# Optimization experiments

Measured on AMD Instinct MI355X. Metric: run time of the kernel, lower is better.

Reference implementation:

```python
import jax, jax.numpy as jnp
import numpy as np
from jax import lax

D_MODEL = 96; D_STATE = 16; D_INNER = 192; DT_RANK = 6; K = 4
BSZ = 2; HH = 64; WW = 64


def setup_inputs() -> dict:
    key = jax.random.key(0)
    ks = jax.random.split(key, 16)
    f = lambda k, shape, s=0.02: (jax.random.normal(k, shape) * s).astype(jnp.float32)
    P = DT_RANK + 2 * D_STATE
    return {
        "x": jax.random.normal(ks[0], (BSZ, HH, WW, D_MODEL), jnp.float32),
        "W_in": f(ks[1], (2 * D_INNER, D_MODEL)),
        "b_in": jnp.zeros((2 * D_INNER,), jnp.float32),
        "conv_w": f(ks[2], (D_INNER, 1, 3, 3)),
        "conv_b": jnp.zeros((D_INNER,), jnp.float32),
        "W_xp": f(ks[3], (K * P, K * D_INNER)),
        "b_xp": jnp.zeros((K * P,), jnp.float32),
        "W_dt": f(ks[4], (K * D_INNER, K * DT_RANK)),
        "b_dt": f(ks[5], (K * D_INNER,), 0.1),
        "A_log": jax.random.normal(ks[6], (K * D_INNER, D_STATE), jnp.float32),
        "D_skip": jnp.ones((K * D_INNER,), jnp.float32),
        "dt_bias": jax.random.normal(ks[7], (K * D_INNER,), jnp.float32),
        "W_out": f(ks[8], (D_MODEL, D_INNER)),
        "b_out": jnp.zeros((D_MODEL,), jnp.float32),
        "gamma": jnp.ones((D_INNER,), jnp.float32),
        "beta": jnp.zeros((D_INNER,), jnp.float32),
    }


def cross_scan(x):
    # x: (B, D, H, W) -> (B, 4, D, L); dirs: row-major, col-major, and their reverses
    B, D, H, W = x.shape
    L = H * W
    x0 = x.reshape(B, D, L)
    x1 = jnp.swapaxes(x, 2, 3).reshape(B, D, L)
    return jnp.stack([x0, x1, x0[..., ::-1], x1[..., ::-1]], axis=1)


def cross_merge(ys):
    # ys: (B, 4, D, H, W) -> (B, D, L); inverse of cross_scan, summed
    B, Kk, D, H, W = ys.shape
    L = H * W
    yf = ys.reshape(B, Kk, D, L)
    y02 = yf[:, 0] + yf[:, 2, :, ::-1]
    y13 = yf[:, 1] + yf[:, 3, :, ::-1]
    y13 = jnp.swapaxes(y13.reshape(B, D, W, H), 2, 3).reshape(B, D, L)
    return y02 + y13


def selective_scan(u, dt, A, Bm, Cm, D_skip, dt_bias):
    # u, dt: (B,K,Dv,L); A: (K,Dv,N); Bm, Cm: (B,K,N,L); D_skip, dt_bias: (K,Dv)
    # NOTE: torch code repeats Bm/Cm across Dv; we broadcast instead (same math).
    dt = jax.nn.softplus(dt + dt_bias[None, :, :, None])
    dt_l = jnp.moveaxis(dt, -1, 0)   # (L,B,K,Dv)
    u_l = jnp.moveaxis(u, -1, 0)     # (L,B,K,Dv)
    B_l = jnp.moveaxis(Bm, -1, 0)    # (L,B,K,N)
    C_l = jnp.moveaxis(Cm, -1, 0)    # (L,B,K,N)

    def step(h, inp):
        dt_t, u_t, b_t, c_t = inp
        dA = jnp.exp(dt_t[..., None] * A[None])                 # (B,K,Dv,N)
        dBu = (dt_t * u_t)[..., None] * b_t[:, :, None, :]      # (B,K,Dv,N)
        h = dA * h + dBu
        y = jnp.einsum('bkdn,bkn->bkd', h, c_t)
        return h, y

    h0 = jnp.zeros(u.shape[:3] + (A.shape[-1],), u.dtype)
    _, ys = lax.scan(step, h0, (dt_l, u_l, B_l, C_l))
    ys = jnp.moveaxis(ys, 0, -1)  # (B,K,Dv,L)
    return ys + u * D_skip[None, :, :, None]


def reference(x, W_in, b_in, conv_w, conv_b, W_xp, b_xp, W_dt, b_dt,
              A_log, D_skip, dt_bias, W_out, b_out, gamma, beta):
    B, H, W, _ = x.shape
    L = H * W
    xz = x @ W_in.T + b_in
    xx, z = jnp.split(xz, 2, axis=-1)
    z = jax.nn.silu(z)
    xc = jnp.transpose(xx, (0, 3, 1, 2))  # (B, D, H, W)
    xc = lax.conv_general_dilated(xc, conv_w, (1, 1), 'SAME',
                                  feature_group_count=D_INNER,
                                  dimension_numbers=('NCHW', 'OIHW', 'NCHW'))
    xc = jax.nn.silu(xc + conv_b[None, :, None, None])

    xs = cross_scan(xc)                      # (B, K, D, L)
    xs_flat = xs.reshape(B, K * D_INNER, L)

    x_dbl = jnp.einsum('bcl,pc->bpl', xs_flat, W_xp) + b_xp[None, :, None]
    x_dbl = x_dbl.reshape(B, K, DT_RANK + 2 * D_STATE, L)
    dts, Bm, Cm = jnp.split(x_dbl, [DT_RANK, DT_RANK + D_STATE], axis=2)
    dts = dts.reshape(B, K * DT_RANK, L)
    dts = jnp.einsum('brl,dr->bdl', dts, W_dt) + b_dt[None, :, None]

    A = -jnp.exp(A_log).reshape(K, D_INNER, D_STATE)
    u = xs_flat.reshape(B, K, D_INNER, L)
    dt = dts.reshape(B, K, D_INNER, L)
    ys = selective_scan(u, dt, A, Bm, Cm,
                        D_skip.reshape(K, D_INNER), dt_bias.reshape(K, D_INNER))

    y = cross_merge(ys.reshape(B, K, D_INNER, H, W))  # (B, D, L)
    y = jnp.transpose(y.reshape(B, D_INNER, H, W), (0, 2, 3, 1))

    mu = jnp.mean(y, axis=-1, keepdims=True)
    var = jnp.mean(jnp.square(y - mu), axis=-1, keepdims=True)
    y = (y - mu) * lax.rsqrt(var + 1e-5) * gamma + beta
    y = y * z
    return y @ W_out.T + b_out
```

## Files before the change

### kernel.cpp

```cpp
#include <hip/hip_runtime.h>
#include <cstdint>
#include <cstddef>


#define CHUNK 16
#define NCK   256

#if __has_builtin(__builtin_amdgcn_exp2f)
#define EXP2(x) __builtin_amdgcn_exp2f(x)
#else
#define EXP2(x) exp2f(x)
#endif
#define LOG2E 1.44269504088896340736f
#define LN2   0.69314718055994530942f

typedef __attribute__((ext_vector_type(8))) short short8;
typedef __attribute__((ext_vector_type(8))) unsigned short ushort8;
typedef __attribute__((ext_vector_type(4))) float f32x4;

__device__ __forceinline__ float siluf(float x){ return x * (1.f/(1.f+__expf(-x))); }
__device__ __forceinline__ float softplus_fast(float v){
  float e  = EXP2(v*LOG2E);
  float sp = LN2*__log2f(1.f + e);
  return (v > 20.f) ? v : sp;
}
__device__ __forceinline__ unsigned short f2b(float f){
  uint32_t u = __float_as_uint(f);
  uint32_t r = (u + 0x7fffu + ((u>>16)&1u)) >> 16;
  return (unsigned short)r;
}
__device__ __forceinline__ short8 cast8(const float* p){
  float4 f0 = *(const float4*)p;
  float4 f1 = *(const float4*)(p+4);
  unsigned short t[8] = {f2b(f0.x),f2b(f0.y),f2b(f0.z),f2b(f0.w),
                         f2b(f1.x),f2b(f1.y),f2b(f1.z),f2b(f1.w)};
  return *(short8*)t;
}

__global__ __launch_bounds__(256) void k_pack(
    const float* __restrict__ Wxp, const float* __restrict__ Win,
    const float* __restrict__ Wout, const float* __restrict__ Wdt,
    unsigned short* __restrict__ Wf, unsigned short* __restrict__ Wfin,
    unsigned short* __restrict__ Wfout, unsigned short* __restrict__ Wdtf)
{
  int tid = blockIdx.x*256 + threadIdx.x;
  int lane = tid & 63;
  int n = lane & 15, q = lane >> 4;
  if (tid < 18432){
    int rest = tid >> 6;
    int pt = rest % 6; rest /= 6;
    int k32 = rest & 3; rest >>= 2;
    int kc = rest % 6; int ph = rest / 6;
    int p = ph*96 + pt*16 + n;
    int kbase = kc*128 + k32*32 + q*8;
    unsigned short v[8];
#pragma unroll
    for (int j = 0; j < 8; j++)
      v[j] = (p < 152) ? f2b(Wxp[(size_t)p*768 + kbase + j]) : (unsigned short)0;
    *(ushort8*)(Wf + (size_t)tid*8) = *(ushort8*)v;
  } else if (tid < 23040){
    int e = tid - 18432;
    int rest = e >> 6;
    int nt = rest % 24, k32 = rest / 24;
    int p = nt*16 + n;
    int kbase = k32*32 + q*8;
    unsigned short v[8];
#pragma unroll
    for (int j = 0; j < 8; j++) v[j] = f2b(Win[(size_t)p*96 + kbase + j]);
    *(ushort8*)(Wfin + (size_t)e*8) = *(ushort8*)v;
  } else if (tid < 25344){
    int e = tid - 23040;
    int rest = e >> 6;
    int nt = rest % 6, k32 = rest / 6;
    int p = nt*16 + n;
    int kbase = k32*32 + q*8;
    unsigned short v[8];
#pragma unroll
    for (int j = 0; j < 8; j++) v[j] = f2b(Wout[(size_t)p*192 + kbase + j]);
    *(ushort8*)(Wfout + (size_t)e*8) = *(ushort8*)v;
  } else if (tid < 28416){
    int e = tid - 25344;
    int nt = e >> 6;
    int ch = nt*16 + n;
    unsigned short v[8];
#pragma unroll
    for (int j = 0; j < 8; j++){
      int kk = q*8 + j;
      v[j] = (kk < 24) ? f2b(Wdt[(size_t)ch*24 + kk]) : (unsigned short)0;
    }
    *(ushort8*)(Wdtf + (size_t)e*8) = *(ushort8*)v;
  }
}

__global__ __launch_bounds__(256) void k_gemm_in(
    const float* __restrict__ x, const unsigned short* __restrict__ Wfin,
    const float* __restrict__ bias, float* __restrict__ xx, float* __restrict__ zs)
{
  const int tid = threadIdx.x;
  const int lane = tid & 63, w = tid >> 6;
  const int m0 = blockIdx.x*64;
  const int n = lane & 15, q = lane >> 4;
  f32x4 acc[4][6] = {};
#pragma unroll
  for (int k32 = 0; k32 < 3; k32++){
    int kb = k32*32 + q*8;
    short8 a[4];
#pragma unroll
    for (int mf = 0; mf < 4; mf++)
      a[mf] = cast8(x + (size_t)(m0 + mf*16 + n)*96 + kb);
#pragma unroll
    for (int j = 0; j < 6; j++){
      int nt = w*6 + j;
      short8 bfr = *(const short8*)(Wfin + ((size_t)(k32*24 + nt)*64 + lane)*8);
#pragma unroll
      for (int mf = 0; mf < 4; mf++)
        acc[mf][j] = __builtin_amdgcn_mfma_f32_16x16x32_bf16(a[mf], bfr, acc[mf][j], 0, 0, 0);
    }
  }
#pragma unroll
  for (int mf = 0; mf < 4; mf++)
#pragma unroll
    for (int j = 0; j < 6; j++){
      int nn = w*96 + j*16 + n;
      float bv = bias[nn];
#pragma unroll
      for (int reg = 0; reg < 4; reg++){
        int l = m0 + mf*16 + q*4 + reg;
        float v = acc[mf][j][reg] + bv;
        if (nn < 192) xx[(size_t)l*192 + nn] = v;
        else          zs[(size_t)l*192 + (nn-192)] = siluf(v);
      }
    }
}

__global__ __launch_bounds__(256) void k_conv(
    const float* __restrict__ xx, const float* __restrict__ cw, const float* __restrict__ cb,
    float* __restrict__ xc,
    unsigned short* __restrict__ xcb, unsigned short* __restrict__ xcTb)
{
  int gid = blockIdx.x*256 + threadIdx.x;
  int c = gid % 192;
  int l = (gid/192) & 4095;
  int b = gid / (192*4096);
  int h = l >> 6, w = l & 63;
  float s = 0.f;
#pragma unroll
  for (int kh = 0; kh < 3; kh++){
    int h2 = h + kh - 1;
    if ((unsigned)h2 >= 64u) continue;
#pragma unroll
    for (int kw = 0; kw < 3; kw++){
      int w2 = w + kw - 1;
      if ((unsigned)w2 >= 64u) continue;
      s += xx[((size_t)b*4096 + h2*64 + w2)*192 + c] * cw[c*9 + kh*3 + kw];
    }
  }
  s = siluf(s + cb[c]);
  unsigned short sb = f2b(s);
  size_t i0 = ((size_t)b*4096 + l)*192 + c;
  xc[i0] = s; xcb[i0] = sb;
  int tl = (l & 63)*64 + (l >> 6);
  xcTb[((size_t)b*4096 + tl)*192 + c] = sb;
}

__global__ __launch_bounds__(256) void k_gemm_xdbl(
    const unsigned short* __restrict__ xcb, const unsigned short* __restrict__ xcTb,
    const unsigned short* __restrict__ Wf, const float* __restrict__ bxp,
    float* __restrict__ xdbl, float* __restrict__ dts_c)
{
  __shared__ unsigned short Bsh[4*6*64*8];
  const int tid = threadIdx.x;
  const int lane = tid & 63, w = tid >> 6;
  const int wl = w & 1, wp = w >> 1;
  const int l0 = blockIdx.x*64, ph = blockIdx.y, b = blockIdx.z;
  const int n = lane & 15, q = lane >> 4;
  f32x4 acc[2][3] = {};
  const unsigned short* slab0 = Wf + (size_t)ph*6*12288;
  for (int kc = 0; kc < 6; kc++){
    __syncthreads();
    const ushort8* srcp = (const ushort8*)(slab0 + (size_t)kc*12288);
#pragma unroll
    for (int t = 0; t < 6; t++) ((ushort8*)Bsh)[tid + t*256] = srcp[tid + t*256];
    __syncthreads();
#pragma unroll
    for (int k32 = 0; k32 < 4; k32++){
      int kk = kc*128 + k32*32;
      int dir = kk/192; int ch = kk%192 + q*8;
      const unsigned short* sp = (dir & 1) ? xcTb : xcb;
      bool rev = (dir >= 2);
      short8 a[2];
#pragma unroll
      for (int mt = 0; mt < 2; mt++){
        int ls = l0 + wl*32 + mt*16 + n;
        int row = rev ? 4095 - ls : ls;
        a[mt] = *(const short8*)(sp + ((size_t)b*4096 + row)*192 + ch);
      }
#pragma unroll
      for (int j = 0; j < 3; j++){
        short8 bfr = *(const short8*)&Bsh[((size_t)(k32*6 + wp*3 + j)*64 + lane)*8];
#pragma unroll
        for (int mt = 0; mt < 2; mt++)
          acc[mt][j] = __builtin_amdgcn_mfma_f32_16x16x32_bf16(a[mt], bfr, acc[mt][j], 0, 0, 0);
      }
    }
  }
#pragma unroll
  for (int mt = 0; mt < 2; mt++)
#pragma unroll
    for (int j = 0; j < 3; j++){
      int p = ph*96 + (wp*3+j)*16 + n;
      if (p < 152){
        int k = p/38, pp = p%38;
        int off = (pp < 6) ? pp : pp + 2;
        float bias = bxp[p];
#pragma unroll
        for (int reg = 0; reg < 4; reg++){
          int l = l0 + wl*32 + mt*16 + q*4 + reg;
          float val = acc[mt][j][reg] + bias;
          xdbl[(((size_t)b*4 + k)*4096 + l)*48 + off] = val;
          if (pp < 6) dts_c[((size_t)b*4096 + l)*24 + k*6 + pp] = val;
        }
      }
    }
}

__global__ __launch_bounds__(256) void k_gemm_dt(
    const float* __restrict__ dts_c, const unsigned short* __restrict__ Wdtf,
    const float* __restrict__ bdt, const float* __restrict__ dtbias,
    float* __restrict__ dte)
{
  const int tid = threadIdx.x;
  const int lane = tid & 63, w = tid >> 6;
  const int m0 = blockIdx.x*64 + w*16;
  const int kdir = blockIdx.y;
  const int n = lane & 15, q = lane >> 4;
  short8 a;
  if (q < 3) a = cast8(dts_c + (size_t)(m0 + n)*24 + q*8);
  else { unsigned short z[8] = {0,0,0,0,0,0,0,0}; a = *(short8*)z; }
  f32x4 acc[12] = {};
#pragma unroll
  for (int j = 0; j < 12; j++){
    int nt = kdir*12 + j;
    short8 bfr = *(const short8*)(Wdtf + ((size_t)nt*64 + lane)*8);
    acc[j] = __builtin_amdgcn_mfma_f32_16x16x32_bf16(a, bfr, acc[j], 0, 0, 0);
  }
#pragma unroll
  for (int j = 0; j < 12; j++){
    int c = j*16 + n;
    int ch = kdir*192 + c;
    float bsum = bdt[ch] + dtbias[ch];
#pragma unroll
    for (int reg = 0; reg < 4; reg++){
      int m = m0 + q*4 + reg;
      int b = m >> 12, l = m & 4095;
      dte[(((size_t)b*4 + kdir)*4096 + l)*192 + c] = softplus_fast(acc[j][reg] + bsum);
    }
  }
}

__global__ __launch_bounds__(256) void k_scanA(
    const float* __restrict__ xc, const float* __restrict__ xdbl,
    const float* __restrict__ A_log, const float* __restrict__ dte,
    float* __restrict__ Pb, float* __restrict__ Sb)
{
  const int lane = threadIdx.x & 63;
  const int wid  = __builtin_amdgcn_readfirstlane(blockIdx.x*4 + (threadIdx.x >> 6));
  const int ck = wid & (NCK-1); const int g = wid / NCK;
  const int dblk = g % 3; const int bk = g / 3;
  const int k = bk & 3; const int b = bk >> 2;
  const int d = dblk*64 + lane; const int ch = k*192 + d;
  float An[16];
  {
    const float4* ap = (const float4*)(A_log + (size_t)ch*16);
#pragma unroll
    for (int i = 0; i < 4; i++){
      float4 t = ap[i];
      An[4*i+0] = -LOG2E*__expf(t.x); An[4*i+1] = -LOG2E*__expf(t.y);
      An[4*i+2] = -LOG2E*__expf(t.z); An[4*i+3] = -LOG2E*__expf(t.w);
    }
  }
  const int l0 = ck*CHUNK;
  const bool rev = (k >= 2);
  const int tr = k & 1;
  const int T0 = tr ? ((l0 & 63)*64 + (l0 >> 6)) : l0;
  const int rs = tr ? 64 : 1;
  const int row0 = rev ? 4095 - T0 : T0;
  const int rstep = (rev ? -rs : rs)*192;
  const float* up  = xc + ((size_t)b*4096 + row0)*192 + d;
  const float* xbc = xdbl + (((size_t)b*4 + k)*4096 + l0)*48;
  const float* dtp = dte + (((size_t)b*4 + k)*4096 + l0)*192 + d;
  float h[16];
#pragma unroll
  for (int n = 0; n < 16; n++) h[n] = 0.f;
  float sdt = 0.f;
#pragma unroll 4
  for (int t = 0; t < CHUNK; t++){
    float u  = up[0];
    float dt = dtp[0];
    float4 B0 = *(const float4*)(xbc + 8);
    float4 B1 = *(const float4*)(xbc + 12);
    float4 B2 = *(const float4*)(xbc + 16);
    float4 B3 = *(const float4*)(xbc + 20);
    float Bv[16] = {B0.x,B0.y,B0.z,B0.w, B1.x,B1.y,B1.z,B1.w,
                    B2.x,B2.y,B2.z,B2.w, B3.x,B3.y,B3.z,B3.w};
    float dtu = dt*u;
    sdt += dt;
#pragma unroll
    for (int n = 0; n < 16; n++){
      float dA = EXP2(dt*An[n]);
      h[n] = fmaf(dA, h[n], dtu*Bv[n]);
    }
    xbc += 48; dtp += 192; up += rstep;
  }
  size_t base = ((size_t)wid*16)*64 + lane;
#pragma unroll
  for (int n = 0; n < 16; n++){
    Pb[base + n*64] = EXP2(An[n]*sdt);
    Sb[base + n*64] = h[n];
  }
}

__global__ __launch_bounds__(64) void k_scanB(
    const float* __restrict__ Pb, const float* __restrict__ Sb, float* __restrict__ H0)
{
  int tid = blockIdx.x*64 + threadIdx.x;
  int lane = tid & 63; int n = (tid >> 6) & 15; int g = tid >> 10;
  float h = 0.f;
#pragma unroll 8
  for (int ck = 0; ck < NCK; ck++){
    size_t idx = (((size_t)(g*NCK + ck)*16) + n)*64 + lane;
    H0[idx] = h;
    h = fmaf(Pb[idx], h, Sb[idx]);
  }
}

__global__ __launch_bounds__(256) void k_scanC(
    const float* __restrict__ xc, const float* __restrict__ xdbl,
    const float* __restrict__ A_log, const float* __restrict__ dte,
    const float* __restrict__ Dskip,
    const float* __restrict__ H0, float* __restrict__ ys)
{
  const int lane = threadIdx.x & 63;
  const int wid  = __builtin_amdgcn_readfirstlane(blockIdx.x*4 + (threadIdx.x >> 6));
  const int ck = wid & (NCK-1); const int g = wid / NCK;
  const int dblk = g % 3; const int bk = g / 3;
  const int k = bk & 3; const int b = bk >> 2;
  const int d = dblk*64 + lane; const int ch = k*192 + d;
  float An[16];
  {
    const float4* ap = (const float4*)(A_log + (size_t)ch*16);
#pragma unroll
    for (int i = 0; i < 4; i++){
      float4 t = ap[i];
      An[4*i+0] = -LOG2E*__expf(t.x); An[4*i+1] = -LOG2E*__expf(t.y);
      An[4*i+2] = -LOG2E*__expf(t.z); An[4*i+3] = -LOG2E*__expf(t.w);
    }
  }
  const float Dv = Dskip[ch];
  const int l0 = ck*CHUNK;
  const bool rev = (k >= 2);
  const int tr = k & 1;
  const int T0 = tr ? ((l0 & 63)*64 + (l0 >> 6)) : l0;
  const int rs = tr ? 64 : 1;
  const int row0 = rev ? 4095 - T0 : T0;
  const int rstep = (rev ? -rs : rs)*192;
  const float* up  = xc + ((size_t)b*4096 + row0)*192 + d;
  const float* xbc = xdbl + (((size_t)b*4 + k)*4096 + l0)*48;
  const float* dtp = dte + (((size_t)b*4 + k)*4096 + l0)*192 + d;
  float* ysp = ys + ((size_t)(k*2 + b))*4096*192 + (size_t)row0*192 + d;
  float h[16];
  size_t base = ((size_t)wid*16)*64 + lane;
#pragma unroll
  for (int n = 0; n < 16; n++) h[n] = H0[base + n*64];
#pragma unroll 4
  for (int t = 0; t < CHUNK; t++){
    float u  = up[0];
    float dt = dtp[0];
    float4 B0 = *(const float4*)(xbc + 8);
    float4 B1 = *(const float4*)(xbc + 12);
    float4 B2 = *(const float4*)(xbc + 16);
    float4 B3 = *(const float4*)(xbc + 20);
    float4 C0 = *(const float4*)(xbc + 24);
    float4 C1 = *(const float4*)(xbc + 28);
    float4 C2 = *(const float4*)(xbc + 32);
    float4 C3 = *(const float4*)(xbc + 36);
    float Bv[16] = {B0.x,B0.y,B0.z,B0.w, B1.x,B1.y,B1.z,B1.w,
                    B2.x,B2.y,B2.z,B2.w, B3.x,B3.y,B3.z,B3.w};
    float Cv[16] = {C0.x,C0.y,C0.z,C0.w, C1.x,C1.y,C1.z,C1.w,
                    C2.x,C2.y,C2.z,C2.w, C3.x,C3.y,C3.z,C3.w};
    float dtu = dt*u;
    float y0 = u*Dv, y1 = 0.f;
#pragma unroll
    for (int n = 0; n < 16; n += 2){
      float dA0 = EXP2(dt*An[n]);
      float dA1 = EXP2(dt*An[n+1]);
      h[n]   = fmaf(dA0, h[n],   dtu*Bv[n]);
      h[n+1] = fmaf(dA1, h[n+1], dtu*Bv[n+1]);
      y0 = fmaf(h[n],   Cv[n],   y0);
      y1 = fmaf(h[n+1], Cv[n+1], y1);
    }
    ysp[0] = y0 + y1;
    xbc += 48; dtp += 192; up += rstep; ysp += rstep;
  }
}

__global__ __launch_bounds__(256) void k_ln(
    const float* __restrict__ ys, const float* __restrict__ zs,
    const float* __restrict__ gamma, const float* __restrict__ beta,
    float* __restrict__ yln)
{
  int row = blockIdx.x*4 + (threadIdx.x >> 6);
  int lane = threadIdx.x & 63;
  int b = row >> 12; int l = row & 4095;
  float v[3];
#pragma unroll
  for (int j = 0; j < 3; j++){
    int c = lane + j*64;
    float s = 0.f;
#pragma unroll
    for (int k = 0; k < 4; k++) s += ys[(((size_t)k*2 + b)*4096 + l)*192 + c];
    v[j] = s;
  }
  float tot = v[0] + v[1] + v[2];
#pragma unroll
  for (int o = 1; o < 64; o <<= 1) tot += __shfl_xor(tot, o);
  float mean = tot * (1.f/192.f);
  float d0 = v[0]-mean, d1 = v[1]-mean, d2 = v[2]-mean;
  float vs = d0*d0 + d1*d1 + d2*d2;
#pragma unroll
  for (int o = 1; o < 64; o <<= 1) vs += __shfl_xor(vs, o);
  float rstd = rsqrtf(vs*(1.f/192.f) + 1e-5f);
  float nd[3] = {d0, d1, d2};
#pragma unroll
  for (int j = 0; j < 3; j++){
    int c = lane + j*64;
    float val = nd[j]*rstd*gamma[c] + beta[c];
    val *= zs[(size_t)row*192 + c];
    yln[(size_t)row*192 + c] = val;
  }
}

__global__ __launch_bounds__(256) void k_gemm_out(
    const float* __restrict__ yln, const unsigned short* __restrict__ Wfout,
    const float* __restrict__ bout, float* __restrict__ out)
{
  const int tid = threadIdx.x;
  const int lane = tid & 63, w = tid >> 6;
  const int m0 = blockIdx.x*64 + w*16;
  const int n = lane & 15, q = lane >> 4;
  f32x4 acc[6] = {};
#pragma unroll
  for (int k32 = 0; k32 < 6; k32++){
    int kb = k32*32 + q*8;
    short8 a = cast8(yln + (size_t)(m0 + n)*192 + kb);
#pragma unroll
    for (int j = 0; j < 6; j++){
      short8 bfr = *(const short8*)(Wfout + ((size_t)(k32*6 + j)*64 + lane)*8);
      acc[j] = __builtin_amdgcn_mfma_f32_16x16x32_bf16(a, bfr, acc[j], 0, 0, 0);
    }
  }
#pragma unroll
  for (int j = 0; j < 6; j++){
    int nn = j*16 + n;
    float bv = bout[nn];
#pragma unroll
    for (int reg = 0; reg < 4; reg++){
      int m = m0 + q*4 + reg;
      out[(size_t)m*96 + nn] = acc[j][reg] + bv;
    }
  }
}

extern "C" void kernel_launch(void* const* d_in, const int* in_sizes, int n_in,
                              void* d_out, int out_size, void* d_ws, size_t ws_size,
                              hipStream_t stream)
{
  const float* x      = (const float*)d_in[0];
  const float* W_in   = (const float*)d_in[1];
  const float* b_in   = (const float*)d_in[2];
  const float* conv_w = (const float*)d_in[3];
  const float* conv_b = (const float*)d_in[4];
  const float* W_xp   = (const float*)d_in[5];
  const float* b_xp   = (const float*)d_in[6];
  const float* W_dt   = (const float*)d_in[7];
  const float* b_dt   = (const float*)d_in[8];
  const float* A_log  = (const float*)d_in[9];
  const float* D_skip = (const float*)d_in[10];
  const float* dt_bias= (const float*)d_in[11];
  const float* W_out  = (const float*)d_in[12];
  const float* b_out  = (const float*)d_in[13];
  const float* gamma  = (const float*)d_in[14];
  const float* beta   = (const float*)d_in[15];
  float* out = (float*)d_out;

  float* ws    = (float*)d_ws;
  float* xx    = ws;
  float* zs    = ws + 1572864;
  float* xc    = ws + 3145728;
  float* xdbl  = ws + 4718592;
  float* ysb   = ws + 6291456;
  float* dte   = ws + 12582912;
  float* Pb    = ws + 18874368;
  float* Sb    = ws + 25165824;
  float* H0    = ws + 31457280;
  float* dts_c = ws + 37748736;
  unsigned short* xcb   = (unsigned short*)(ws + 37945344);
  unsigned short* xcTb  = xcb + 1572864;
  unsigned short* Wf    = (unsigned short*)(ws + 39518208);
  unsigned short* Wfin  = (unsigned short*)(ws + 39591936);
  unsigned short* Wfout = (unsigned short*)(ws + 39610368);
  unsigned short* Wdtf  = (unsigned short*)(ws + 39619584);
  float* yln   = ws + 39631872;

  k_pack     <<<111,             256, 0, stream>>>(W_xp, W_in, W_out, W_dt, Wf, Wfin, Wfout, Wdtf);
  k_gemm_in  <<<128,             256, 0, stream>>>(x, Wfin, b_in, xx, zs);
  k_conv     <<<6144,            256, 0, stream>>>(xx, conv_w, conv_b, xc, xcb, xcTb);
  k_gemm_xdbl<<<dim3(64, 2, 2),  256, 0, stream>>>(xcb, xcTb, Wf, b_xp, xdbl, dts_c);
  k_gemm_dt  <<<dim3(128, 4),    256, 0, stream>>>(dts_c, Wdtf, b_dt, dt_bias, dte);
  k_scanA    <<<1536,            256, 0, stream>>>(xc, xdbl, A_log, dte, Pb, Sb);
  k_scanB    <<<384,             64,  0, stream>>>(Pb, Sb, H0);
  k_scanC    <<<1536,            256, 0, stream>>>(xc, xdbl, A_log, dte, D_skip, H0, ysb);
  k_ln       <<<2048,            256, 0, stream>>>(ysb, zs, gamma, beta, yln);
  k_gemm_out <<<128,             256, 0, stream>>>(yln, Wfout, b_out, out);
}
```

Measured before the change: 223.6 us.

## Split scan state dimension across two waves to double scan parallelism

The chunked selective-scan kernels now split the 16 state components into two halves, each handled by a separate wave, doubling the grid to 3072 blocks and halving per-thread register state. Each half writes its own partial output buffer, and the layernorm kernel sums 8 partials instead of 4. The aim is higher occupancy and latency hiding in the scan. The cost is that u, dt and x loads are duplicated, and twice as much ys traffic is written and then read by the layernorm.

```diff
diff --git a/kernel.cpp b/kernel.cpp
--- a/kernel.cpp
+++ b/kernel.cpp
@@ -258,22 +258,23 @@
   }
 }
 
-__global__ __launch_bounds__(256) void k_scanA(
+__global__ __launch_bounds__(256, 8) void k_scanA(
     const float* __restrict__ xc, const float* __restrict__ xdbl,
     const float* __restrict__ A_log, const float* __restrict__ dte,
     float* __restrict__ Pb, float* __restrict__ Sb)
 {
   const int lane = threadIdx.x & 63;
   const int wid  = __builtin_amdgcn_readfirstlane(blockIdx.x*4 + (threadIdx.x >> 6));
-  const int ck = wid & (NCK-1); const int g = wid / NCK;
-  const int dblk = g % 3; const int bk = g / 3;
+  const int ck = wid & (NCK-1); const int g = wid >> 8;
+  const int nh = g & 1; const int gg = g >> 1;
+  const int dblk = gg % 3; const int bk = gg / 3;
   const int k = bk & 3; const int b = bk >> 2;
   const int d = dblk*64 + lane; const int ch = k*192 + d;
-  float An[16];
+  float An[8];
   {
-    const float4* ap = (const float4*)(A_log + (size_t)ch*16);
-#pragma unroll
-    for (int i = 0; i < 4; i++){
+    const float4* ap = (const float4*)(A_log + (size_t)ch*16 + nh*8);
+#pragma unroll
+    for (int i = 0; i < 2; i++){
       float4 t = ap[i];
       An[4*i+0] = -LOG2E*__expf(t.x); An[4*i+1] = -LOG2E*__expf(t.y);
       An[4*i+2] = -LOG2E*__expf(t.z); An[4*i+3] = -LOG2E*__expf(t.w);
@@ -287,11 +288,11 @@
   const int row0 = rev ? 4095 - T0 : T0;
   const int rstep = (rev ? -rs : rs)*192;
   const float* up  = xc + ((size_t)b*4096 + row0)*192 + d;
-  const float* xbc = xdbl + (((size_t)b*4 + k)*4096 + l0)*48;
+  const float* xbc = xdbl + (((size_t)b*4 + k)*4096 + l0)*48 + nh*8;
   const float* dtp = dte + (((size_t)b*4 + k)*4096 + l0)*192 + d;
-  float h[16];
-#pragma unroll
-  for (int n = 0; n < 16; n++) h[n] = 0.f;
+  float h[8];
+#pragma unroll
+  for (int n = 0; n < 8; n++) h[n] = 0.f;
   float sdt = 0.f;
 #pragma unroll 4
   for (int t = 0; t < CHUNK; t++){
@@ -299,22 +300,19 @@
     float dt = dtp[0];
     float4 B0 = *(const float4*)(xbc + 8);
     float4 B1 = *(const float4*)(xbc + 12);
-    float4 B2 = *(const float4*)(xbc + 16);
-    float4 B3 = *(const float4*)(xbc + 20);
-    float Bv[16] = {B0.x,B0.y,B0.z,B0.w, B1.x,B1.y,B1.z,B1.w,
-                    B2.x,B2.y,B2.z,B2.w, B3.x,B3.y,B3.z,B3.w};
+    float Bv[8] = {B0.x,B0.y,B0.z,B0.w, B1.x,B1.y,B1.z,B1.w};
     float dtu = dt*u;
     sdt += dt;
 #pragma unroll
-    for (int n = 0; n < 16; n++){
+    for (int n = 0; n < 8; n++){
       float dA = EXP2(dt*An[n]);
       h[n] = fmaf(dA, h[n], dtu*Bv[n]);
     }
     xbc += 48; dtp += 192; up += rstep;
   }
-  size_t base = ((size_t)wid*16)*64 + lane;
-#pragma unroll
-  for (int n = 0; n < 16; n++){
+  size_t base = ((size_t)wid*8)*64 + lane;
+#pragma unroll
+  for (int n = 0; n < 8; n++){
     Pb[base + n*64] = EXP2(An[n]*sdt);
     Sb[base + n*64] = h[n];
   }
@@ -324,17 +322,17 @@
     const float* __restrict__ Pb, const float* __restrict__ Sb, float* __restrict__ H0)
 {
   int tid = blockIdx.x*64 + threadIdx.x;
-  int lane = tid & 63; int n = (tid >> 6) & 15; int g = tid >> 10;
+  int lane = tid & 63; int n = (tid >> 6) & 7; int g = tid >> 9;
   float h = 0.f;
 #pragma unroll 8
   for (int ck = 0; ck < NCK; ck++){
-    size_t idx = (((size_t)(g*NCK + ck)*16) + n)*64 + lane;
+    size_t idx = (((size_t)(g*NCK + ck)*8) + n)*64 + lane;
     H0[idx] = h;
     h = fmaf(Pb[idx], h, Sb[idx]);
   }
 }
 
-__global__ __launch_bounds__(256) void k_scanC(
+__global__ __launch_bounds__(256, 8) void k_scanC(
     const float* __restrict__ xc, const float* __restrict__ xdbl,
     const float* __restrict__ A_log, const float* __restrict__ dte,
     const float* __restrict__ Dskip,
@@ -342,21 +340,22 @@
 {
   const int lane = threadIdx.x & 63;
   const int wid  = __builtin_amdgcn_readfirstlane(blockIdx.x*4 + (threadIdx.x >> 6));
-  const int ck = wid & (NCK-1); const int g = wid / NCK;
-  const int dblk = g % 3; const int bk = g / 3;
+  const int ck = wid & (NCK-1); const int g = wid >> 8;
+  const int nh = g & 1; const int gg = g >> 1;
+  const int dblk = gg % 3; const int bk = gg / 3;
   const int k = bk & 3; const int b = bk >> 2;
   const int d = dblk*64 + lane; const int ch = k*192 + d;
-  float An[16];
+  float An[8];
   {
-    const float4* ap = (const float4*)(A_log + (size_t)ch*16);
-#pragma unroll
-    for (int i = 0; i < 4; i++){
+    const float4* ap = (const float4*)(A_log + (size_t)ch*16 + nh*8);
+#pragma unroll
+    for (int i = 0; i < 2; i++){
       float4 t = ap[i];
       An[4*i+0] = -LOG2E*__expf(t.x); An[4*i+1] = -LOG2E*__expf(t.y);
       An[4*i+2] = -LOG2E*__expf(t.z); An[4*i+3] = -LOG2E*__expf(t.w);
     }
   }
-  const float Dv = Dskip[ch];
+  const float Dv = (nh == 0) ? Dskip[ch] : 0.f;
   const int l0 = ck*CHUNK;
   const bool rev = (k >= 2);
   const int tr = k & 1;
@@ -365,33 +364,27 @@
   const int row0 = rev ? 4095 - T0 : T0;
   const int rstep = (rev ? -rs : rs)*192;
   const float* up  = xc + ((size_t)b*4096 + row0)*192 + d;
-  const float* xbc = xdbl + (((size_t)b*4 + k)*4096 + l0)*48;
+  const float* xbc = xdbl + (((size_t)b*4 + k)*4096 + l0)*48 + nh*8;
   const float* dtp = dte + (((size_t)b*4 + k)*4096 + l0)*192 + d;
-  float* ysp = ys + ((size_t)(k*2 + b))*4096*192 + (size_t)row0*192 + d;
-  float h[16];
-  size_t base = ((size_t)wid*16)*64 + lane;
-#pragma unroll
-  for (int n = 0; n < 16; n++) h[n] = H0[base + n*64];
+  float* ysp = ys + ((size_t)((k*2 + b)*2 + nh))*4096*192 + (size_t)row0*192 + d;
+  float h[8];
+  size_t base = ((size_t)wid*8)*64 + lane;
+#pragma unroll
+  for (int n = 0; n < 8; n++) h[n] = H0[base + n*64];
 #pragma unroll 4
   for (int t = 0; t < CHUNK; t++){
     float u  = up[0];
     float dt = dtp[0];
     float4 B0 = *(const float4*)(xbc + 8);
     float4 B1 = *(const float4*)(xbc + 12);
-    float4 B2 = *(const float4*)(xbc + 16);
-    float4 B3 = *(const float4*)(xbc + 20);
     float4 C0 = *(const float4*)(xbc + 24);
     float4 C1 = *(const float4*)(xbc + 28);
-    float4 C2 = *(const float4*)(xbc + 32);
-    float4 C3 = *(const float4*)(xbc + 36);
-    float Bv[16] = {B0.x,B0.y,B0.z,B0.w, B1.x,B1.y,B1.z,B1.w,
-                    B2.x,B2.y,B2.z,B2.w, B3.x,B3.y,B3.z,B3.w};
-    float Cv[16] = {C0.x,C0.y,C0.z,C0.w, C1.x,C1.y,C1.z,C1.w,
-                    C2.x,C2.y,C2.z,C2.w, C3.x,C3.y,C3.z,C3.w};
+    float Bv[8] = {B0.x,B0.y,B0.z,B0.w, B1.x,B1.y,B1.z,B1.w};
+    float Cv[8] = {C0.x,C0.y,C0.z,C0.w, C1.x,C1.y,C1.z,C1.w};
     float dtu = dt*u;
     float y0 = u*Dv, y1 = 0.f;
 #pragma unroll
-    for (int n = 0; n < 16; n += 2){
+    for (int n = 0; n < 8; n += 2){
       float dA0 = EXP2(dt*An[n]);
       float dA1 = EXP2(dt*An[n+1]);
       h[n]   = fmaf(dA0, h[n],   dtu*Bv[n]);
@@ -418,7 +411,10 @@
     int c = lane + j*64;
     float s = 0.f;
 #pragma unroll
-    for (int k = 0; k < 4; k++) s += ys[(((size_t)k*2 + b)*4096 + l)*192 + c];
+    for (int k = 0; k < 4; k++)
+#pragma unroll
+      for (int nh = 0; nh < 2; nh++)
+        s += ys[(((size_t)((k*2 + b)*2 + nh))*4096 + l)*192 + c];
     v[j] = s;
   }
   float tot = v[0] + v[1] + v[2];
@@ -499,27 +495,27 @@
   float* xc    = ws + 3145728;
   float* xdbl  = ws + 4718592;
   float* ysb   = ws + 6291456;
-  float* dte   = ws + 12582912;
-  float* Pb    = ws + 18874368;
-  float* Sb    = ws + 25165824;
-  float* H0    = ws + 31457280;
-  float* dts_c = ws + 37748736;
-  unsigned short* xcb   = (unsigned short*)(ws + 37945344);
+  float* dte   = ws + 18874368;
+  float* Pb    = ws + 25165824;
+  float* Sb    = ws + 31457280;
+  float* H0    = ws + 37748736;
+  float* dts_c = ws + 44040192;
+  unsigned short* xcb   = (unsigned short*)(ws + 44236800);
   unsigned short* xcTb  = xcb + 1572864;
-  unsigned short* Wf    = (unsigned short*)(ws + 39518208);
-  unsigned short* Wfin  = (unsigned short*)(ws + 39591936);
-  unsigned short* Wfout = (unsigned short*)(ws + 39610368);
-  unsigned short* Wdtf  = (unsigned short*)(ws + 39619584);
-  float* yln   = ws + 39631872;
+  unsigned short* Wf    = (unsigned short*)(ws + 45809664);
+  unsigned short* Wfin  = (unsigned short*)(ws + 45883392);
+  unsigned short* Wfout = (unsigned short*)(ws + 45901824);
+  unsigned short* Wdtf  = (unsigned short*)(ws + 45911040);
+  float* yln   = ws + 45923328;
 
   k_pack     <<<111,             256, 0, stream>>>(W_xp, W_in, W_out, W_dt, Wf, Wfin, Wfout, Wdtf);
   k_gemm_in  <<<128,             256, 0, stream>>>(x, Wfin, b_in, xx, zs);
   k_conv     <<<6144,            256, 0, stream>>>(xx, conv_w, conv_b, xc, xcb, xcTb);
   k_gemm_xdbl<<<dim3(64, 2, 2),  256, 0, stream>>>(xcb, xcTb, Wf, b_xp, xdbl, dts_c);
   k_gemm_dt  <<<dim3(128, 4),    256, 0, stream>>>(dts_c, Wdtf, b_dt, dt_bias, dte);
-  k_scanA    <<<1536,            256, 0, stream>>>(xc, xdbl, A_log, dte, Pb, Sb);
+  k_scanA    <<<3072,            256, 0, stream>>>(xc, xdbl, A_log, dte, Pb, Sb);
   k_scanB    <<<384,             64,  0, stream>>>(Pb, Sb, H0);
-  k_scanC    <<<1536,            256, 0, stream>>>(xc, xdbl, A_log, dte, D_skip, H0, ysb);
+  k_scanC    <<<3072,            256, 0, stream>>>(xc, xdbl, A_log, dte, D_skip, H0, ysb);
   k_ln       <<<2048,            256, 0, stream>>>(ysb, zs, gamma, beta, yln);
   k_gemm_out <<<128,             256, 0, stream>>>(yln, Wfout, b_out, out);
 }
```

Result: no change. 225.8 us (+1.0%).
